# Kernel optimization log

Hardware: AMD Instinct MI355X
Metric: run time of the kernel (lower is better)

Reference implementation:

```python
import jax, jax.numpy as jnp
import numpy as np

HEADS = 8
IN_CH = 768
INNER = 768
DK = INNER // HEADS


def setup_inputs() -> dict:
    key = jax.random.key(0)
    ks = jax.random.split(key, 9)
    bs, hw = 16, 1024
    s = 1.0 / np.sqrt(IN_CH)
    sp = 1.0 / np.sqrt(INNER)
    return {
        "x": jax.random.normal(ks[0], (bs, hw, IN_CH), jnp.float32),
        # weights stored (in, out) so y = x @ W + b (equiv to torch Linear)
        "Wq": jax.random.uniform(ks[1], (IN_CH, INNER), jnp.float32, -s, s),
        "bq": jax.random.uniform(ks[2], (INNER,), jnp.float32, -s, s),
        "Wk": jax.random.uniform(ks[3], (IN_CH, INNER), jnp.float32, -s, s),
        "bk": jax.random.uniform(ks[4], (INNER,), jnp.float32, -s, s),
        "Wv": jax.random.uniform(ks[5], (IN_CH, INNER), jnp.float32, -s, s),
        "bv": jax.random.uniform(ks[6], (INNER,), jnp.float32, -s, s),
        "Wp": jax.random.uniform(ks[7], (INNER, IN_CH), jnp.float32, -sp, sp),
        "bp": jax.random.uniform(ks[8], (IN_CH,), jnp.float32, -sp, sp),
    }


def reference(x, Wq, bq, Wk, bk, Wv, bv, Wp, bp):
    bs, hw, _ = x.shape
    # NOTE: the original torch code does .view(bs, heads, hw, dk) on a
    # (bs, hw, inner) tensor — a raw row-major reshape, not a head-split
    # transpose. Replicate exactly.
    q = (x @ Wq + bq).reshape(bs, HEADS, hw, DK)
    k = (x @ Wk + bk).reshape(bs, HEADS, hw, DK)
    v = (x @ Wv + bv).reshape(bs, HEADS, hw, DK)
    logits = jnp.einsum("bhqd,bhkd->bhqk", q, k) / np.sqrt(DK).astype(np.float32)
    attn = jax.nn.softmax(logits, axis=-1)
    out = jnp.einsum("bhqk,bhkd->bhqd", attn, v).reshape(bs, hw, INNER)
    # dropout is identity in eval mode
    return out @ Wp + bp
```

## Files before the change

### kernel.cpp

```cpp
#include <hip/hip_runtime.h>
#include <math.h>

typedef __bf16 bf16;
typedef __attribute__((ext_vector_type(8))) __bf16 bf16x8;
typedef __attribute__((ext_vector_type(4))) __bf16 bf16x4;
typedef __attribute__((ext_vector_type(4))) float f32x4;
typedef __attribute__((ext_vector_type(16))) float f32x16;

#define CE 0.14724445f
#define THR_RAW 54.0f

#define GLOAD16(g, l)                                                          \
    __builtin_amdgcn_global_load_lds(                                          \
        (const __attribute__((address_space(1))) void*)(g),                    \
        (__attribute__((address_space(3))) void*)(l), 16, 0, 0)

__global__ __launch_bounds__(256) void cvt_x(const float* __restrict__ x, bf16* __restrict__ xb) {
    size_t i = ((size_t)blockIdx.x * 256 + threadIdx.x) * 4;
    f32x4 v = *(const f32x4*)(x + i);
    bf16x4 o;
    o[0] = (bf16)v[0]; o[1] = (bf16)v[1]; o[2] = (bf16)v[2]; o[3] = (bf16)v[3];
    *(bf16x4*)(xb + i) = o;
}

struct WArgs { const float* w[4]; };

__global__ __launch_bounds__(256) void transpose_w(WArgs wa, bf16* __restrict__ out) {
    __shared__ float t[32][33];
    const int z = blockIdx.z;
    const float* __restrict__ W = wa.w[z];
    bf16* __restrict__ Wt = out + (size_t)z * 589824;
    int k0 = blockIdx.x * 32, n0 = blockIdx.y * 32;
    int tx = threadIdx.x, ty = threadIdx.y;
#pragma unroll
    for (int j = 0; j < 4; ++j)
        t[ty + j * 8][tx] = W[(size_t)(k0 + ty + j * 8) * 768 + n0 + tx];
    __syncthreads();
#pragma unroll
    for (int j = 0; j < 4; ++j)
        Wt[(size_t)(n0 + ty + j * 8) * 768 + k0 + tx] = (bf16)t[tx][ty + j * 8];
}

struct GemmArgs {
    const bf16* Bt[3];
    const float* bias[3];
    void* out[3];
};

template <bool F32OUT>
__global__ __launch_bounds__(256, 2) void gemm_kernel(const bf16* __restrict__ A, GemmArgs ga) {
    __shared__ __align__(16) bf16 As[128 * 64];
    __shared__ __align__(16) bf16 Bs[128 * 64];
    const int nwg = gridDim.x;
    const int bid = blockIdx.x;
    const int lid = (bid & 7) * (nwg >> 3) + (bid >> 3);
    const int z = lid / 768;
    const int rem = lid - z * 768;
    const int m0 = (rem / 6) * 128;
    const int n0 = (rem % 6) * 128;
    const bf16* __restrict__ Bt = ga.Bt[z];
    const int tid = threadIdx.x;
    const int lane = tid & 63, l15 = lane & 15, lq = lane >> 4;
    const int wid = tid >> 6;
    const int wm = (wid >> 1) * 64, wn = (wid & 1) * 64;

    const bf16* asrc[4]; const bf16* bsrc[4]; bf16* adst[4]; bf16* bdst[4];
#pragma unroll
    for (int i = 0; i < 4; ++i) {
        int r = (wid * 4 + i) * 8 + (lane >> 3);
        int s = lane & 7;
        int c = s ^ (r & 7);
        asrc[i] = A + (size_t)(m0 + r) * 768 + c * 8;
        bsrc[i] = Bt + (size_t)(n0 + r) * 768 + c * 8;
        adst[i] = As + (wid * 4 + i) * 512;
        bdst[i] = Bs + (wid * 4 + i) * 512;
    }

    f32x4 acc[4][4] = {};

    for (int ks = 0; ks < 768; ks += 64) {
#pragma unroll
        for (int i = 0; i < 4; ++i) {
            GLOAD16(asrc[i] + ks, adst[i]);
            GLOAD16(bsrc[i] + ks, bdst[i]);
        }
        __syncthreads();
#pragma unroll
        for (int kk = 0; kk < 2; ++kk) {
            bf16x8 af[4], bfr[4];
#pragma unroll
            for (int f = 0; f < 4; ++f) {
                int ar = wm + f * 16 + l15;
                int ac = (kk * 4 + lq) ^ (ar & 7);
                af[f] = *(const bf16x8*)(As + ar * 64 + ac * 8);
                int br = wn + f * 16 + l15;
                int bc = (kk * 4 + lq) ^ (br & 7);
                bfr[f] = *(const bf16x8*)(Bs + br * 64 + bc * 8);
            }
#pragma unroll
            for (int mf = 0; mf < 4; ++mf)
#pragma unroll
                for (int nf = 0; nf < 4; ++nf)
                    acc[mf][nf] = __builtin_amdgcn_mfma_f32_16x16x32_bf16(af[mf], bfr[nf], acc[mf][nf], 0, 0, 0);
        }
        __syncthreads();
    }
    const float* __restrict__ bias = ga.bias[z];
#pragma unroll
    for (int nf = 0; nf < 4; ++nf) {
        int col = n0 + wn + nf * 16 + l15;
        float bv = bias[col];
#pragma unroll
        for (int mf = 0; mf < 4; ++mf) {
            int rbase = m0 + wm + mf * 16 + lq * 4;
#pragma unroll
            for (int i = 0; i < 4; ++i) {
                float v = acc[mf][nf][i] + bv;
                if constexpr (F32OUT)
                    ((float*)ga.out[z])[(size_t)(rbase + i) * 768 + col] = v;
                else
                    ((bf16*)ga.out[z])[(size_t)(rbase + i) * 768 + col] = (bf16)v;
            }
        }
    }
}

__global__ __launch_bounds__(256) void transpose_v(const bf16* __restrict__ V, bf16* __restrict__ Vt) {
    __shared__ unsigned short t[64 * 97];
    const int g = blockIdx.y;
    const int kv0 = blockIdx.x * 64;
    const unsigned short* __restrict__ Vg = (const unsigned short*)V + (size_t)g * 98304;
    unsigned short* __restrict__ Vtg = (unsigned short*)Vt + (size_t)g * 98304;
    const int tid = threadIdx.x;
#pragma unroll
    for (int p = 0; p < 24; ++p) {
        int id = tid + p * 256;
        int row = id / 96, col = id % 96;
        t[row * 97 + col] = Vg[(size_t)(kv0 + row) * 96 + col];
    }
    __syncthreads();
#pragma unroll
    for (int p = 0; p < 24; ++p) {
        int id = tid + p * 256;
        int d = id >> 6, j = id & 63;
        Vtg[(size_t)d * 1024 + kv0 + j] = t[j * 97 + d];
    }
}

static __device__ inline int pk2(float a, float b) {
    union { __bf16 h[2]; int w; } u;
    u.h[0] = (__bf16)a; u.h[1] = (__bf16)b;
    return u.w;
}

static __device__ inline bf16x8 pack_step(float p0, float p1, float p2, float p3,
                                          float p4, float p5, float p6, float p7, int hi) {
    int A0 = pk2(p0, p1), A1 = pk2(p2, p3);
    int B0 = pk2(p4, p5), B1 = pk2(p6, p7);
    int t0 = hi ? A0 : B0;
    int t1 = hi ? A1 : B1;
    int x0 = __shfl_xor(t0, 32);
    int x1 = __shfl_xor(t1, 32);
    union { int w[4]; bf16x8 v; } u;
    u.w[0] = hi ? x0 : A0;
    u.w[1] = hi ? x1 : A1;
    u.w[2] = hi ? B0 : x0;
    u.w[3] = hi ? B1 : x1;
    return u.v;
}

__global__ __launch_bounds__(256, 3) void attn_kernel(const bf16* __restrict__ Q, const bf16* __restrict__ K,
                                                      const bf16* __restrict__ Vt, bf16* __restrict__ AO) {
    __shared__ __align__(16) bf16 Ks[64 * 128];
    __shared__ __align__(16) bf16 Vss[2 * 96 * 64];
    const int g = blockIdx.x;
    const int q0 = blockIdx.y * 128;
    const int tid = threadIdx.x;
    const int lane = tid & 63;
    const int l31 = lane & 31, hi = lane >> 5, wid = tid >> 6;
    const int sw = l31 & 7;
    const int qrow = q0 + wid * 32 + l31;
    const size_t gbase = (size_t)g * 98304;
    const bf16* __restrict__ Qg = Q + gbase;
    const bf16* __restrict__ Kg = K + gbase;
    const bf16* __restrict__ Vg = Vt + gbase;
    bf16* __restrict__ Og = AO + gbase;

    const bf16* ksrc[4]; bf16* kdst[4];
#pragma unroll
    for (int i = 0; i < 4; ++i) {
        int r = (wid * 4 + i) * 4 + (lane >> 4);
        int s = lane & 15;
        int c = s ^ (r & 7);
        ksrc[i] = Kg + r * 96 + c * 8;
        kdst[i] = Ks + (wid * 4 + i) * 512;
    }
    const bf16* vsrc[3]; int vdoff[3];
#pragma unroll
    for (int i = 0; i < 3; ++i) {
        int r = (wid * 3 + i) * 8 + (lane >> 3);
        int s = lane & 7;
        int c = s ^ (r & 7);
        vsrc[i] = Vg + (size_t)r * 1024 + c * 8;
        vdoff[i] = (wid * 3 + i) * 512;
    }

    bf16x8 qf[6];
#pragma unroll
    for (int kk = 0; kk < 6; ++kk)
        qf[kk] = *(const bf16x8*)(Qg + (size_t)qrow * 96 + kk * 16 + hi * 8);

#pragma unroll
    for (int i = 0; i < 4; ++i) GLOAD16(ksrc[i], kdst[i]);
#pragma unroll
    for (int i = 0; i < 3; ++i) GLOAD16(vsrc[i], Vss + vdoff[i]);
    __syncthreads();
#pragma unroll
    for (int i = 0; i < 3; ++i) GLOAD16(vsrc[i] + 64, Vss + 6144 + vdoff[i]);

    f32x16 o[3] = {};
    float mrun = -INFINITY, lrun = 0.f;

    for (int kt = 0; kt < 16; ++kt) {
        const bf16* Vcur = Vss + (kt & 1) * 6144;

        f32x16 s0 = {}, s1 = {};
        __builtin_amdgcn_s_setprio(1);
#pragma unroll
        for (int kk = 0; kk < 6; ++kk) {
            int slot = ((kk * 2 + hi) ^ sw) * 8;
            bf16x8 k0 = *(const bf16x8*)(Ks + l31 * 128 + slot);
            bf16x8 k1 = *(const bf16x8*)(Ks + (l31 + 32) * 128 + slot);
            s0 = __builtin_amdgcn_mfma_f32_32x32x16_bf16(k0, qf[kk], s0, 0, 0, 0);
            s1 = __builtin_amdgcn_mfma_f32_32x32x16_bf16(k1, qf[kk], s1, 0, 0, 0);
        }
        __builtin_amdgcn_s_setprio(0);
        __syncthreads();
        if (kt < 15) {
#pragma unroll
            for (int i = 0; i < 4; ++i) GLOAD16(ksrc[i] + (kt + 1) * 6144, kdst[i]);
        }

        float t0 = fmaxf(fmaxf(s0[0], s0[1]), fmaxf(s0[2], s0[3]));
        float t1 = fmaxf(fmaxf(s0[4], s0[5]), fmaxf(s0[6], s0[7]));
        float t2 = fmaxf(fmaxf(s0[8], s0[9]), fmaxf(s0[10], s0[11]));
        float t3 = fmaxf(fmaxf(s0[12], s0[13]), fmaxf(s0[14], s0[15]));
        float u0 = fmaxf(fmaxf(s1[0], s1[1]), fmaxf(s1[2], s1[3]));
        float u1 = fmaxf(fmaxf(s1[4], s1[5]), fmaxf(s1[6], s1[7]));
        float u2 = fmaxf(fmaxf(s1[8], s1[9]), fmaxf(s1[10], s1[11]));
        float u3 = fmaxf(fmaxf(s1[12], s1[13]), fmaxf(s1[14], s1[15]));
        float pmax = fmaxf(fmaxf(fmaxf(t0, t1), fmaxf(t2, t3)),
                           fmaxf(fmaxf(u0, u1), fmaxf(u2, u3)));
        pmax = fmaxf(pmax, __shfl_xor(pmax, 32));
        if (!__all(pmax - mrun <= THR_RAW)) {
            float newm = fmaxf(mrun, pmax);
            float alpha = __builtin_amdgcn_exp2f(CE * (mrun - newm));
            mrun = newm;
            lrun *= alpha;
#pragma unroll
            for (int df = 0; df < 3; ++df)
#pragma unroll
                for (int r = 0; r < 16; ++r) o[df][r] *= alpha;
        }
        float lsa = 0.f, lsb = 0.f;
#pragma unroll
        for (int r = 0; r < 16; ++r) {
            float p = __builtin_amdgcn_exp2f(CE * (s0[r] - mrun));
            s0[r] = p; lsa += p;
        }
#pragma unroll
        for (int r = 0; r < 16; ++r) {
            float p = __builtin_amdgcn_exp2f(CE * (s1[r] - mrun));
            s1[r] = p; lsb += p;
        }
        float lsum = lsa + lsb;
        lsum += __shfl_xor(lsum, 32);
        lrun += lsum;

        bf16x8 pb0 = pack_step(s0[0], s0[1], s0[2], s0[3], s0[4], s0[5], s0[6], s0[7], hi);
        bf16x8 pb1 = pack_step(s0[8], s0[9], s0[10], s0[11], s0[12], s0[13], s0[14], s0[15], hi);
        bf16x8 pb2 = pack_step(s1[0], s1[1], s1[2], s1[3], s1[4], s1[5], s1[6], s1[7], hi);
        bf16x8 pb3 = pack_step(s1[8], s1[9], s1[10], s1[11], s1[12], s1[13], s1[14], s1[15], hi);
        __builtin_amdgcn_s_setprio(1);
#pragma unroll
        for (int df = 0; df < 3; ++df) {
            const bf16* vrow = Vcur + (df * 32 + l31) * 64;
            bf16x8 v0 = *(const bf16x8*)(vrow + ((0 + hi) ^ sw) * 8);
            bf16x8 v1 = *(const bf16x8*)(vrow + ((2 + hi) ^ sw) * 8);
            bf16x8 v2 = *(const bf16x8*)(vrow + ((4 + hi) ^ sw) * 8);
            bf16x8 v3 = *(const bf16x8*)(vrow + ((6 + hi) ^ sw) * 8);
            o[df] = __builtin_amdgcn_mfma_f32_32x32x16_bf16(v0, pb0, o[df], 0, 0, 0);
            o[df] = __builtin_amdgcn_mfma_f32_32x32x16_bf16(v1, pb1, o[df], 0, 0, 0);
            o[df] = __builtin_amdgcn_mfma_f32_32x32x16_bf16(v2, pb2, o[df], 0, 0, 0);
            o[df] = __builtin_amdgcn_mfma_f32_32x32x16_bf16(v3, pb3, o[df], 0, 0, 0);
        }
        __builtin_amdgcn_s_setprio(0);
        __syncthreads();
        if (kt < 14) {
#pragma unroll
            for (int i = 0; i < 3; ++i)
                GLOAD16(vsrc[i] + (kt + 2) * 64, Vss + (kt & 1) * 6144 + vdoff[i]);
        }
    }

    float inv = 1.0f / lrun;
#pragma unroll
    for (int df = 0; df < 3; ++df)
#pragma unroll
        for (int rq = 0; rq < 4; ++rq) {
            bf16x4 ov;
#pragma unroll
            for (int j = 0; j < 4; ++j) ov[j] = (bf16)(o[df][rq * 4 + j] * inv);
            *(bf16x4*)(Og + (size_t)qrow * 96 + df * 32 + rq * 8 + hi * 4) = ov;
        }
}

extern "C" void kernel_launch(void* const* d_in, const int* in_sizes, int n_in,
                              void* d_out, int out_size, void* d_ws, size_t ws_size,
                              hipStream_t stream) {
    const float* x  = (const float*)d_in[0];
    const float* Wq = (const float*)d_in[1];
    const float* bq = (const float*)d_in[2];
    const float* Wk = (const float*)d_in[3];
    const float* bk = (const float*)d_in[4];
    const float* Wv = (const float*)d_in[5];
    const float* bv = (const float*)d_in[6];
    const float* Wp = (const float*)d_in[7];
    const float* bp = (const float*)d_in[8];

    char* ws = (char*)d_ws;
    bf16* xb  = (bf16*)(ws);
    bf16* wt  = (bf16*)(ws + 25165824);
    bf16* Qb  = (bf16*)(ws + 29884416);
    bf16* Kb  = (bf16*)(ws + 55050240);
    bf16* Vb  = (bf16*)(ws + 80216064);
    bf16* Vtb = (bf16*)(ws + 105381888);
    bf16* AO  = xb;

    cvt_x<<<12288, 256, 0, stream>>>(x, xb);

    WArgs wa;
    wa.w[0] = Wq; wa.w[1] = Wk; wa.w[2] = Wv; wa.w[3] = Wp;
    transpose_w<<<dim3(24, 24, 4), dim3(32, 8), 0, stream>>>(wa, wt);

    GemmArgs g1{};
    g1.Bt[0] = wt;            g1.Bt[1] = wt + 589824;  g1.Bt[2] = wt + 2 * 589824;
    g1.bias[0] = bq;          g1.bias[1] = bk;         g1.bias[2] = bv;
    g1.out[0] = Qb;           g1.out[1] = Kb;          g1.out[2] = Vb;
    gemm_kernel<false><<<2304, 256, 0, stream>>>(xb, g1);

    transpose_v<<<dim3(16, 128), 256, 0, stream>>>(Vb, Vtb);

    attn_kernel<<<dim3(128, 8), 256, 0, stream>>>(Qb, Kb, Vtb, AO);

    GemmArgs g2{};
    g2.Bt[0] = wt + 3 * 589824; g2.bias[0] = bp; g2.out[0] = (void*)d_out;
    g2.Bt[1] = g2.Bt[0]; g2.Bt[2] = g2.Bt[0];
    g2.bias[1] = bp; g2.bias[2] = bp;
    g2.out[1] = g2.out[0]; g2.out[2] = g2.out[0];
    gemm_kernel<true><<<768, 256, 0, stream>>>(AO, g2);
}
```

Baseline: 197.2 us.

## Use slot-major LDS layout for K/V tiles and reorder QKV GEMM tile mapping

```diff
diff --git a/kernel.cpp b/kernel.cpp
--- a/kernel.cpp
+++ b/kernel.cpp
@@ -47,17 +47,19 @@
     void* out[3];
 };
 
-template <bool F32OUT>
+template <bool F32OUT, int NZ>
 __global__ __launch_bounds__(256, 2) void gemm_kernel(const bf16* __restrict__ A, GemmArgs ga) {
     __shared__ __align__(16) bf16 As[128 * 64];
     __shared__ __align__(16) bf16 Bs[128 * 64];
     const int nwg = gridDim.x;
     const int bid = blockIdx.x;
     const int lid = (bid & 7) * (nwg >> 3) + (bid >> 3);
-    const int z = lid / 768;
-    const int rem = lid - z * 768;
-    const int m0 = (rem / 6) * 128;
-    const int n0 = (rem % 6) * 128;
+    const int mt = lid / (6 * NZ);
+    const int r0 = lid - mt * (6 * NZ);
+    const int z  = r0 / 6;
+    const int nt = r0 - z * 6;
+    const int m0 = mt * 128;
+    const int n0 = nt * 128;
     const bf16* __restrict__ Bt = ga.Bt[z];
     const int tid = threadIdx.x;
     const int lane = tid & 63, l15 = lane & 15, lq = lane >> 4;
@@ -171,14 +173,13 @@
 
 __global__ __launch_bounds__(256, 3) void attn_kernel(const bf16* __restrict__ Q, const bf16* __restrict__ K,
                                                       const bf16* __restrict__ Vt, bf16* __restrict__ AO) {
-    __shared__ __align__(16) bf16 Ks[64 * 128];
-    __shared__ __align__(16) bf16 Vss[2 * 96 * 64];
+    __shared__ __align__(16) bf16 Ks[12 * 64 * 8];
+    __shared__ __align__(16) bf16 Vss[2 * 8 * 96 * 8];
     const int g = blockIdx.x;
     const int q0 = blockIdx.y * 128;
     const int tid = threadIdx.x;
     const int lane = tid & 63;
     const int l31 = lane & 31, hi = lane >> 5, wid = tid >> 6;
-    const int sw = l31 & 7;
     const int qrow = q0 + wid * 32 + l31;
     const size_t gbase = (size_t)g * 98304;
     const bf16* __restrict__ Qg = Q + gbase;
@@ -186,22 +187,19 @@
     const bf16* __restrict__ Vg = Vt + gbase;
     bf16* __restrict__ Og = AO + gbase;
 
-    const bf16* ksrc[4]; bf16* kdst[4];
-#pragma unroll
-    for (int i = 0; i < 4; ++i) {
-        int r = (wid * 4 + i) * 4 + (lane >> 4);
-        int s = lane & 15;
-        int c = s ^ (r & 7);
-        ksrc[i] = Kg + r * 96 + c * 8;
-        kdst[i] = Ks + (wid * 4 + i) * 512;
+    const bf16* ksrc[3]; bf16* kdst[3];
+#pragma unroll
+    for (int i = 0; i < 3; ++i) {
+        int slot = wid * 3 + i;
+        ksrc[i] = Kg + (size_t)lane * 96 + slot * 8;
+        kdst[i] = Ks + slot * 512;
     }
     const bf16* vsrc[3]; int vdoff[3];
 #pragma unroll
     for (int i = 0; i < 3; ++i) {
-        int r = (wid * 3 + i) * 8 + (lane >> 3);
-        int s = lane & 7;
-        int c = s ^ (r & 7);
-        vsrc[i] = Vg + (size_t)r * 1024 + c * 8;
+        int f = (wid * 3 + i) * 64 + lane;
+        int slot = f / 96, row = f - slot * 96;
+        vsrc[i] = Vg + (size_t)row * 1024 + slot * 8;
         vdoff[i] = (wid * 3 + i) * 512;
     }
 
@@ -211,7 +209,7 @@
         qf[kk] = *(const bf16x8*)(Qg + (size_t)qrow * 96 + kk * 16 + hi * 8);
 
 #pragma unroll
-    for (int i = 0; i < 4; ++i) GLOAD16(ksrc[i], kdst[i]);
+    for (int i = 0; i < 3; ++i) GLOAD16(ksrc[i], kdst[i]);
 #pragma unroll
     for (int i = 0; i < 3; ++i) GLOAD16(vsrc[i], Vss + vdoff[i]);
     __syncthreads();
@@ -221,16 +219,17 @@
     f32x16 o[3] = {};
     float mrun = -INFINITY, lrun = 0.f;
 
+    const bf16* kbase = Ks + hi * 512 + l31 * 8;
+
     for (int kt = 0; kt < 16; ++kt) {
-        const bf16* Vcur = Vss + (kt & 1) * 6144;
+        const bf16* vbase = Vss + (kt & 1) * 6144 + hi * 768 + l31 * 8;
 
         f32x16 s0 = {}, s1 = {};
         __builtin_amdgcn_s_setprio(1);
 #pragma unroll
         for (int kk = 0; kk < 6; ++kk) {
-            int slot = ((kk * 2 + hi) ^ sw) * 8;
-            bf16x8 k0 = *(const bf16x8*)(Ks + l31 * 128 + slot);
-            bf16x8 k1 = *(const bf16x8*)(Ks + (l31 + 32) * 128 + slot);
+            bf16x8 k0 = *(const bf16x8*)(kbase + kk * 1024);
+            bf16x8 k1 = *(const bf16x8*)(kbase + kk * 1024 + 256);
             s0 = __builtin_amdgcn_mfma_f32_32x32x16_bf16(k0, qf[kk], s0, 0, 0, 0);
             s1 = __builtin_amdgcn_mfma_f32_32x32x16_bf16(k1, qf[kk], s1, 0, 0, 0);
         }
@@ -238,7 +237,7 @@
         __syncthreads();
         if (kt < 15) {
 #pragma unroll
-            for (int i = 0; i < 4; ++i) GLOAD16(ksrc[i] + (kt + 1) * 6144, kdst[i]);
+            for (int i = 0; i < 3; ++i) GLOAD16(ksrc[i] + (kt + 1) * 6144, kdst[i]);
         }
 
         float t0 = fmaxf(fmaxf(s0[0], s0[1]), fmaxf(s0[2], s0[3]));
@@ -284,11 +283,10 @@
         __builtin_amdgcn_s_setprio(1);
 #pragma unroll
         for (int df = 0; df < 3; ++df) {
-            const bf16* vrow = Vcur + (df * 32 + l31) * 64;
-            bf16x8 v0 = *(const bf16x8*)(vrow + ((0 + hi) ^ sw) * 8);
-            bf16x8 v1 = *(const bf16x8*)(vrow + ((2 + hi) ^ sw) * 8);
-            bf16x8 v2 = *(const bf16x8*)(vrow + ((4 + hi) ^ sw) * 8);
-            bf16x8 v3 = *(const bf16x8*)(vrow + ((6 + hi) ^ sw) * 8);
+            bf16x8 v0 = *(const bf16x8*)(vbase + 0 * 1536 + df * 256);
+            bf16x8 v1 = *(const bf16x8*)(vbase + 1 * 1536 + df * 256);
+            bf16x8 v2 = *(const bf16x8*)(vbase + 2 * 1536 + df * 256);
+            bf16x8 v3 = *(const bf16x8*)(vbase + 3 * 1536 + df * 256);
             o[df] = __builtin_amdgcn_mfma_f32_32x32x16_bf16(v0, pb0, o[df], 0, 0, 0);
             o[df] = __builtin_amdgcn_mfma_f32_32x32x16_bf16(v1, pb1, o[df], 0, 0, 0);
             o[df] = __builtin_amdgcn_mfma_f32_32x32x16_bf16(v2, pb2, o[df], 0, 0, 0);
@@ -347,7 +345,7 @@
     g1.Bt[0] = wt;            g1.Bt[1] = wt + 589824;  g1.Bt[2] = wt + 2 * 589824;
     g1.bias[0] = bq;          g1.bias[1] = bk;         g1.bias[2] = bv;
     g1.out[0] = Qb;           g1.out[1] = Kb;          g1.out[2] = Vb;
-    gemm_kernel<false><<<2304, 256, 0, stream>>>(xb, g1);
+    gemm_kernel<false, 3><<<2304, 256, 0, stream>>>(xb, g1);
 
     transpose_v<<<dim3(16, 128), 256, 0, stream>>>(Vb, Vtb);
 
@@ -358,5 +356,5 @@
     g2.Bt[1] = g2.Bt[0]; g2.Bt[2] = g2.Bt[0];
     g2.bias[1] = bp; g2.bias[2] = bp;
     g2.out[1] = g2.out[0]; g2.out[2] = g2.out[0];
-    gemm_kernel<true><<<768, 256, 0, stream>>>(AO, g2);
-}
+    gemm_kernel<true, 1><<<768, 256, 0, stream>>>(AO, g2);
+}
```

After: 199.4 us. Within noise of the previous version (+1.1%).
